# Kernel tuning notes

Hardware: AMD Instinct MI355X
Metric: run time of the kernel (lower is better)

Reference implementation:

```python
import jax, jax.numpy as jnp
import numpy as np

HIDDEN = 1024
HEADS = 16
HEAD_DIM = HIDDEN // HEADS


def setup_inputs() -> dict:
    key = jax.random.key(0)
    kx, kq, kk, kv, ko = jax.random.split(key, 5)
    s = 1.0 / np.sqrt(HIDDEN)
    return {
        "x": jax.random.normal(kx, (2, 2048, HIDDEN), dtype=jnp.float32),
        "Wq": jax.random.normal(kq, (HIDDEN, HIDDEN), dtype=jnp.float32) * s,
        "Wk": jax.random.normal(kk, (HIDDEN, HIDDEN), dtype=jnp.float32) * s,
        "Wv": jax.random.normal(kv, (HIDDEN, HIDDEN), dtype=jnp.float32) * s,
        "Wo": jax.random.normal(ko, (HIDDEN, HIDDEN), dtype=jnp.float32) * s,
    }


def reference(x, Wq, Wk, Wv, Wo):
    B, T, C = x.shape
    H, D = HEADS, HEAD_DIM
    # projections (torch Linear: y = x @ W.T); weights here stored as (out,in)==(C,C)
    q = (x @ Wq.T).reshape(B, T, H, D)
    k = (x @ Wk.T).reshape(B, T, H, D)
    v = (x @ Wv.T).reshape(B, T, H, D)
    scale = 1.0 / np.sqrt(D).astype(np.float32)
    # scores: (B,H,T,T)
    attn = jnp.einsum("bqhd,bkhd->bhqk", q, k) * scale
    causal = jnp.tril(jnp.ones((T, T), dtype=bool))  # keep lower triangle
    attn = jnp.where(causal, attn, -jnp.inf)
    attn = jax.nn.softmax(attn, axis=-1)
    out = jnp.einsum("bhqk,bkhd->bqhd", attn, v).reshape(B, T, C)
    return out @ Wo.T
```

## Files before the change

kernel.cpp:

```cpp
#include <hip/hip_runtime.h>
#include <cstdint>
#include <cstddef>

#define HID 1024
#define NH 16
#define HD 64
#define SEQ 2048
#define BATCH 2

typedef __attribute__((ext_vector_type(8))) short bf16x8;
typedef __attribute__((ext_vector_type(4))) short bf16x4;
typedef bf16x8 __attribute__((may_alias)) bf16x8_ma;
typedef bf16x4 __attribute__((may_alias)) bf16x4_ma;
typedef __attribute__((ext_vector_type(4))) float f32x4;

__device__ __forceinline__ unsigned short f2bf(float f){
  unsigned u = __builtin_bit_cast(unsigned, f);
  u += 0x7fffu + ((u >> 16) & 1u);
  return (unsigned short)(u >> 16);
}

__device__ __forceinline__ unsigned cvtpk_bf16(float lo, float hi){
  unsigned r;
  asm("v_cvt_pk_bf16_f32 %0, %1, %2" : "=v"(r) : "v"(lo), "v"(hi));
  return r;
}

__device__ __forceinline__ void gll(const unsigned short* g, unsigned short* l){
  __builtin_amdgcn_global_load_lds(
      (const __attribute__((address_space(1))) unsigned int*)(g),
      (__attribute__((address_space(3))) unsigned int*)(l),
      16, 0, 0);
}

__global__ __launch_bounds__(256) void cvt_all(
    const float* __restrict__ x,  const float* __restrict__ wq,
    const float* __restrict__ wk, const float* __restrict__ wv,
    const float* __restrict__ wo,
    unsigned short* __restrict__ xb,  unsigned short* __restrict__ wqb,
    unsigned short* __restrict__ wkb, unsigned short* __restrict__ wvb,
    unsigned short* __restrict__ wob)
{
  const size_t NX = (size_t)BATCH*SEQ*HID;
  const size_t NW = (size_t)HID*HID;
  size_t i = ((size_t)blockIdx.x*256 + threadIdx.x)*4;
  const float* src; unsigned short* dst; size_t off;
  if (i < NX) { src = x; dst = xb; off = i; }
  else {
    size_t j = i - NX; int w = (int)(j >> 20); off = j & (NW-1);
    if      (w==0){ src=wq; dst=wqb; }
    else if (w==1){ src=wk; dst=wkb; }
    else if (w==2){ src=wv; dst=wvb; }
    else          { src=wo; dst=wob; }
  }
  float4 v = *(const float4*)(src+off);
  uint2 p;
  p.x = (unsigned)f2bf(v.x) | ((unsigned)f2bf(v.y)<<16);
  p.y = (unsigned)f2bf(v.z) | ((unsigned)f2bf(v.w)<<16);
  *(uint2*)(dst+off) = p;
}

__global__ __launch_bounds__(256) void gemm_qkv(
    const unsigned short* __restrict__ A,
    const unsigned short* __restrict__ Bq,
    const unsigned short* __restrict__ Bk,
    const unsigned short* __restrict__ Bv,
    unsigned short* __restrict__ Qh,
    unsigned short* __restrict__ Kh,
    unsigned short* __restrict__ Vh)
{
  __shared__ unsigned short As[8192];
  __shared__ unsigned short Bs[8192];
  const int tid = threadIdx.x;
  const int w = tid >> 6, lane = tid & 63, l15 = lane & 15, quad = lane >> 4;
  const int wm = (w >> 1)*64, wn = (w & 1)*64;
  const int bm = blockIdx.y*128;
  const int which = blockIdx.x >> 3;
  const int bn = (blockIdx.x & 7)*128;
  const unsigned short* B = which==0 ? Bq : (which==1 ? Bk : Bv);
  unsigned short* C       = which==0 ? Qh : (which==1 ? Kh : Vh);
  const float cscale      = which==0 ? 0.18033688011112042f : 1.0f;
  const int lrow = lane >> 2, lcol = (lane & 3)*8;

  f32x4 acc[4][4] = {};
  for (int kb=0; kb<16; ++kb){
    __syncthreads();
    #pragma unroll
    for (int p=0;p<4;p++){
      int c = p*4 + w;
      int h = c >> 3, rb = c & 7;
      gll(&A[(size_t)(bm + rb*16 + lrow)*HID + kb*64 + h*32 + lcol], &As[h*4096 + rb*512]);
      gll(&B[(size_t)(bn + rb*16 + lrow)*HID + kb*64 + h*32 + lcol], &Bs[h*4096 + rb*512]);
    }
    __syncthreads();
    #pragma unroll
    for (int kc=0;kc<2;kc++){
      bf16x8 af[4], bfr[4];
      #pragma unroll
      for (int i=0;i<4;i++) af[i]  = *(const bf16x8*)(&As[kc*4096 + (wm + i*16 + l15)*32 + quad*8]);
      #pragma unroll
      for (int j=0;j<4;j++) bfr[j] = *(const bf16x8*)(&Bs[kc*4096 + (wn + j*16 + l15)*32 + quad*8]);
      #pragma unroll
      for (int i=0;i<4;i++)
        #pragma unroll
        for (int j=0;j<4;j++)
          acc[i][j] = __builtin_amdgcn_mfma_f32_16x16x32_bf16(af[i], bfr[j], acc[i][j], 0,0,0);
    }
  }
  #pragma unroll
  for (int i=0;i<4;i++)
    #pragma unroll
    for (int j=0;j<4;j++)
      #pragma unroll
      for (int r=0;r<4;r++){
        int m = bm + wm + i*16 + quad*4 + r;
        int n = bn + wn + j*16 + l15;
        int b = m >> 11, t = m & (SEQ-1), h = n >> 6, d = n & (HD-1);
        C[(((size_t)(b*NH + h))*SEQ + t)*HD + d] = f2bf(acc[i][j][r]*cscale);
      }
}

__global__ __launch_bounds__(256) void gemm_out(
    const unsigned short* __restrict__ A,
    const unsigned short* __restrict__ B,
    float* __restrict__ C)
{
  __shared__ unsigned short As[8192];
  __shared__ unsigned short Bs[4096];
  const int tid = threadIdx.x;
  const int w = tid >> 6, lane = tid & 63, l15 = lane & 15, quad = lane >> 4;
  const int wm = (w >> 1)*64, wn = (w & 1)*32;
  const int bm = blockIdx.y*128, bn = blockIdx.x*64;
  const int lrow = lane >> 2, lcol = (lane & 3)*8;

  f32x4 acc[4][2] = {};
  for (int kb=0; kb<16; ++kb){
    __syncthreads();
    #pragma unroll
    for (int p=0;p<4;p++){
      int c = p*4 + w;
      int h = c >> 3, rb = c & 7;
      gll(&A[(size_t)(bm + rb*16 + lrow)*HID + kb*64 + h*32 + lcol], &As[h*4096 + rb*512]);
    }
    #pragma unroll
    for (int p=0;p<2;p++){
      int c = p*4 + w;
      int h = c >> 2, rb = c & 3;
      gll(&B[(size_t)(bn + rb*16 + lrow)*HID + kb*64 + h*32 + lcol], &Bs[h*2048 + rb*512]);
    }
    __syncthreads();
    #pragma unroll
    for (int kc=0;kc<2;kc++){
      bf16x8 af[4], bfr[2];
      #pragma unroll
      for (int i=0;i<4;i++) af[i]  = *(const bf16x8*)(&As[kc*4096 + (wm + i*16 + l15)*32 + quad*8]);
      #pragma unroll
      for (int j=0;j<2;j++) bfr[j] = *(const bf16x8*)(&Bs[kc*2048 + (wn + j*16 + l15)*32 + quad*8]);
      #pragma unroll
      for (int i=0;i<4;i++)
        #pragma unroll
        for (int j=0;j<2;j++)
          acc[i][j] = __builtin_amdgcn_mfma_f32_16x16x32_bf16(af[i], bfr[j], acc[i][j], 0,0,0);
    }
  }
  #pragma unroll
  for (int i=0;i<4;i++)
    #pragma unroll
    for (int j=0;j<2;j++)
      #pragma unroll
      for (int r=0;r<4;r++){
        int m = bm + wm + i*16 + quad*4 + r;
        int n = bn + wn + j*16 + l15;
        C[(size_t)m*HID + n] = acc[i][j][r];
      }
}

__global__ __launch_bounds__(256) void vtrans(
    const unsigned short* __restrict__ Vh, unsigned short* __restrict__ VhT)
{
  __shared__ unsigned short t[64*66];
  const int bh = blockIdx.y, tb = blockIdx.x;
  const int tid = threadIdx.x;
  const unsigned short* src = Vh + ((size_t)bh*SEQ + tb*64)*HD;
  #pragma unroll
  for (int i=0;i<2;i++){
    int c = i*256 + tid; int r = c >> 3, c8 = (c & 7)*8;
    unsigned short tmp[8];
    *(uint4*)tmp = *(const uint4*)(&src[r*HD + c8]);
    #pragma unroll
    for (int j=0;j<8;j++) t[(c8+j)*66 + r] = tmp[j];
  }
  __syncthreads();
  unsigned short* dst = VhT + (size_t)bh*HD*SEQ + tb*64;
  #pragma unroll
  for (int i=0;i<2;i++){
    int c = i*256 + tid; int d = c >> 3, t8 = (c & 7)*8;
    uint4 v; unsigned short* pv = (unsigned short*)&v;
    #pragma unroll
    for (int j=0;j<8;j++) pv[j] = t[d*66 + t8 + j];
    *(uint4*)(&dst[(size_t)d*SEQ + t8]) = v;
  }
}

__global__ __launch_bounds__(256, 4) void attn(
    const unsigned short* __restrict__ Qh,
    const unsigned short* __restrict__ Kh,
    const unsigned short* __restrict__ VhT,
    unsigned short* __restrict__ Ao)
{
  __shared__ unsigned short QP[4096];
  __shared__ unsigned short Ks[2][4096];
  __shared__ unsigned short Vt[2][4096];

  const int bh = blockIdx.x;
  const int y  = blockIdx.y;
  const int a = y & 7, bb = y >> 3;
  const int qb = (bb & 1) ? (7 - a)*4 + bb : a*4 + bb;
  const int tid = threadIdx.x;
  const int w = tid >> 6, lane = tid & 63, l15 = lane & 15, quad = lane >> 4;
  const int lrow = lane >> 2, lcol = (lane & 3)*8;

  const size_t base = (size_t)bh * SEQ * HD;
  const unsigned short* Qg  = Qh + base + (size_t)qb*64*HD;
  const unsigned short* VTg = VhT + base;
  unsigned short* Psw = QP + w*1024;
  const unsigned swz = (unsigned)(l15 & 7) << 4;

  #pragma unroll
  for (int p=0;p<2;p++){
    int c = w*2 + p;
    gll(&Qg[(size_t)((c&3)*16 + lrow)*HD + (c>>2)*32 + lcol], &QP[(c>>2)*2048 + (c&3)*512]);
  }
  {
    const unsigned short* Kg = Kh + base;
    if (w < 2){
      #pragma unroll
      for (int p=0;p<4;p++){ int cc = w*4 + p;
        gll(&Kg[(size_t)((cc&3)*16 + lrow)*HD + (cc>>2)*32 + lcol], &Ks[0][(cc>>2)*2048 + (cc&3)*512]); }
    } else {
      #pragma unroll
      for (int p=0;p<4;p++){ int cc = (w-2)*4 + p;
        gll(&VTg[(size_t)((cc&3)*16 + lrow)*SEQ + (cc>>2)*32 + lcol], &Vt[0][(cc>>2)*2048 + (cc&3)*512]); }
    }
  }
  __syncthreads();
  bf16x8 qfrag[2];
  #pragma unroll
  for (int kc=0;kc<2;kc++)
    qfrag[kc] = *(const bf16x8*)(&QP[kc*2048 + (w*16 + l15)*32 + quad*8]);
  __syncthreads();

  f32x4 lacc = {0.f, 0.f, 0.f, 0.f};
  f32x4 oacc[4] = {};
  const int qrow = qb*64 + w*16 + l15;
  int cur = 0;

  for (int kb=0; kb<=qb; ++kb){
    if (kb < qb){
      const unsigned short* Kg2 = Kh + base + (size_t)(kb+1)*64*HD;
      unsigned short* Kd = Ks[cur^1];
      unsigned short* Vd = Vt[cur^1];
      if (w < 2){
        #pragma unroll
        for (int p=0;p<4;p++){ int cc = w*4 + p;
          gll(&Kg2[(size_t)((cc&3)*16 + lrow)*HD + (cc>>2)*32 + lcol], &Kd[(cc>>2)*2048 + (cc&3)*512]); }
      } else {
        #pragma unroll
        for (int p=0;p<4;p++){ int cc = (w-2)*4 + p;
          gll(&VTg[(size_t)((cc&3)*16 + lrow)*SEQ + (size_t)(kb+1)*64 + (cc>>2)*32 + lcol], &Vd[(cc>>2)*2048 + (cc&3)*512]); }
      }
    }

    const unsigned short* Ksc = Ks[cur];
    f32x4 s[4] = {};
    #pragma unroll
    for (int cb=0;cb<4;cb++)
      #pragma unroll
      for (int kc=0;kc<2;kc++){
        bf16x8 kfr = *(const bf16x8*)(&Ksc[kc*2048 + (cb*16 + l15)*32 + quad*8]);
        s[cb] = __builtin_amdgcn_mfma_f32_16x16x32_bf16(kfr, qfrag[kc], s[cb], 0,0,0);
      }

    if (kb == qb){
      #pragma unroll
      for (int cb=0;cb<4;cb++)
        #pragma unroll
        for (int r=0;r<4;r++){
          int t = kb*64 + cb*16 + quad*4 + r;
          if (t > qrow) s[cb][r] = -1e30f;
        }
    }
    #pragma unroll
    for (int cb=0;cb<4;cb++)
      #pragma unroll
      for (int r=0;r<4;r++)
        s[cb][r] = exp2f(s[cb][r]);
    lacc += (s[0] + s[1]) + (s[2] + s[3]);

    #pragma unroll
    for (int cb=0;cb<4;cb++){
      uint2 d2;
      d2.x = cvtpk_bf16(s[cb][0], s[cb][1]);
      d2.y = cvtpk_bf16(s[cb][2], s[cb][3]);
      *(bf16x4_ma*)((char*)Psw + (((unsigned)(l15*128 + cb*32 + quad*8)) ^ swz)) =
          __builtin_bit_cast(bf16x4, d2);
    }
    asm volatile("" ::: "memory");
    bf16x8 pa[2];
    #pragma unroll
    for (int kc=0;kc<2;kc++)
      pa[kc] = *(const bf16x8_ma*)((const char*)Psw + (((unsigned)(l15*128 + kc*64 + quad*16)) ^ swz));

    const unsigned short* Vtc = Vt[cur];
    #pragma unroll
    for (int db=0;db<4;db++)
      #pragma unroll
      for (int kc=0;kc<2;kc++){
        bf16x8 vfr = *(const bf16x8*)(&Vtc[kc*2048 + (db*16 + l15)*32 + quad*8]);
        oacc[db] = __builtin_amdgcn_mfma_f32_16x16x32_bf16(pa[kc], vfr, oacc[db], 0,0,0);
      }

    if (kb < qb) __syncthreads();
    cur ^= 1;
  }

  float l = (lacc[0] + lacc[1]) + (lacc[2] + lacc[3]);
  l += __shfl_xor(l, 16);
  l += __shfl_xor(l, 32);
  float inv[4];
  #pragma unroll
  for (int r=0;r<4;r++)
    inv[r] = 1.0f / __shfl(l, quad*4 + r);

  const int b = bh >> 4, h = bh & (NH-1);
  #pragma unroll
  for (int db=0;db<4;db++)
    #pragma unroll
    for (int r=0;r<4;r++){
      int t = qb*64 + w*16 + quad*4 + r;
      int col = h*HD + db*16 + l15;
      Ao[((size_t)b*SEQ + t)*HID + col] = f2bf(oacc[db][r] * inv[r]);
    }
}

extern "C" void kernel_launch(void* const* d_in, const int* in_sizes, int n_in,
                              void* d_out, int out_size, void* d_ws, size_t ws_size,
                              hipStream_t stream)
{
  const float* x  = (const float*)d_in[0];
  const float* Wq = (const float*)d_in[1];
  const float* Wk = (const float*)d_in[2];
  const float* Wv = (const float*)d_in[3];
  const float* Wo = (const float*)d_in[4];

  unsigned short* xb  = (unsigned short*)d_ws;
  unsigned short* wqb = xb  + (size_t)4*1024*1024;
  unsigned short* wkb = wqb + (size_t)1024*1024;
  unsigned short* wvb = wkb + (size_t)1024*1024;
  unsigned short* wob = wvb + (size_t)1024*1024;
  unsigned short* Qh  = wob + (size_t)1024*1024;
  unsigned short* Kh  = Qh  + (size_t)4*1024*1024;
  unsigned short* Vh  = Kh  + (size_t)4*1024*1024;
  unsigned short* VhT = Vh  + (size_t)4*1024*1024;
  unsigned short* Ao  = xb;

  cvt_all<<<8192, 256, 0, stream>>>(x, Wq, Wk, Wv, Wo, xb, wqb, wkb, wvb, wob);

  gemm_qkv<<<dim3(24, 32), 256, 0, stream>>>(xb, wqb, wkb, wvb, Qh, Kh, Vh);

  vtrans<<<dim3(SEQ/64, BATCH*NH), 256, 0, stream>>>(Vh, VhT);

  attn<<<dim3(BATCH*NH, SEQ/64), 256, 0, stream>>>(Qh, Kh, VhT, Ao);

  gemm_out<<<dim3(16, 32), 256, 0, stream>>>(Ao, wob, (float*)d_out);
}
```

Measured before the change: 188.8 us.

## Double-buffer QKV GEMM K-loop and stage epilogue through swizzled LDS

After: 181.3 us. 4.0% less time.

```diff
diff --git a/kernel.cpp b/kernel.cpp
--- a/kernel.cpp
+++ b/kernel.cpp
@@ -12,6 +12,7 @@
 typedef __attribute__((ext_vector_type(4))) short bf16x4;
 typedef bf16x8 __attribute__((may_alias)) bf16x8_ma;
 typedef bf16x4 __attribute__((may_alias)) bf16x4_ma;
+typedef uint4 __attribute__((may_alias)) uint4_ma;
 typedef __attribute__((ext_vector_type(4))) float f32x4;
 
 __device__ __forceinline__ unsigned short f2bf(float f){
@@ -69,8 +70,7 @@
     unsigned short* __restrict__ Kh,
     unsigned short* __restrict__ Vh)
 {
-  __shared__ unsigned short As[8192];
-  __shared__ unsigned short Bs[8192];
+  __shared__ unsigned short S[16384];
   const int tid = threadIdx.x;
   const int w = tid >> 6, lane = tid & 63, l15 = lane & 15, quad = lane >> 4;
   const int wm = (w >> 1)*64, wn = (w & 1)*64;
@@ -83,41 +83,69 @@
   const int lrow = lane >> 2, lcol = (lane & 3)*8;
 
   f32x4 acc[4][4] = {};
-  for (int kb=0; kb<16; ++kb){
+
+  {
+    #pragma unroll
+    for (int p=0;p<2;p++){
+      int c = w*2 + p;
+      gll(&A[(size_t)(bm + c*16 + lrow)*HID + lcol], &S[c*512]);
+      gll(&B[(size_t)(bn + c*16 + lrow)*HID + lcol], &S[8192 + c*512]);
+    }
+  }
+  __syncthreads();
+
+  int cur = 0;
+  for (int kb=0; kb<32; ++kb){
+    if (kb < 31){
+      unsigned short* Ad = S + (cur^1)*4096;
+      unsigned short* Bd = S + 8192 + (cur^1)*4096;
+      #pragma unroll
+      for (int p=0;p<2;p++){
+        int c = w*2 + p;
+        gll(&A[(size_t)(bm + c*16 + lrow)*HID + (kb+1)*32 + lcol], &Ad[c*512]);
+        gll(&B[(size_t)(bn + c*16 + lrow)*HID + (kb+1)*32 + lcol], &Bd[c*512]);
+      }
+    }
+    const unsigned short* Ac = S + cur*4096;
+    const unsigned short* Bc = S + 8192 + cur*4096;
+    bf16x8 af[4], bfr[4];
+    #pragma unroll
+    for (int i=0;i<4;i++) af[i]  = *(const bf16x8*)(&Ac[(wm + i*16 + l15)*32 + quad*8]);
+    #pragma unroll
+    for (int j=0;j<4;j++) bfr[j] = *(const bf16x8*)(&Bc[(wn + j*16 + l15)*32 + quad*8]);
+    #pragma unroll
+    for (int i=0;i<4;i++)
+      #pragma unroll
+      for (int j=0;j<4;j++)
+        acc[i][j] = __builtin_amdgcn_mfma_f32_16x16x32_bf16(af[i], bfr[j], acc[i][j], 0,0,0);
     __syncthreads();
-    #pragma unroll
-    for (int p=0;p<4;p++){
-      int c = p*4 + w;
-      int h = c >> 3, rb = c & 7;
-      gll(&A[(size_t)(bm + rb*16 + lrow)*HID + kb*64 + h*32 + lcol], &As[h*4096 + rb*512]);
-      gll(&B[(size_t)(bn + rb*16 + lrow)*HID + kb*64 + h*32 + lcol], &Bs[h*4096 + rb*512]);
-    }
-    __syncthreads();
-    #pragma unroll
-    for (int kc=0;kc<2;kc++){
-      bf16x8 af[4], bfr[4];
-      #pragma unroll
-      for (int i=0;i<4;i++) af[i]  = *(const bf16x8*)(&As[kc*4096 + (wm + i*16 + l15)*32 + quad*8]);
-      #pragma unroll
-      for (int j=0;j<4;j++) bfr[j] = *(const bf16x8*)(&Bs[kc*4096 + (wn + j*16 + l15)*32 + quad*8]);
-      #pragma unroll
-      for (int i=0;i<4;i++)
-        #pragma unroll
-        for (int j=0;j<4;j++)
-          acc[i][j] = __builtin_amdgcn_mfma_f32_16x16x32_bf16(af[i], bfr[j], acc[i][j], 0,0,0);
-    }
-  }
+    cur ^= 1;
+  }
+
   #pragma unroll
   for (int i=0;i<4;i++)
     #pragma unroll
     for (int j=0;j<4;j++)
       #pragma unroll
       for (int r=0;r<4;r++){
-        int m = bm + wm + i*16 + quad*4 + r;
-        int n = bn + wn + j*16 + l15;
-        int b = m >> 11, t = m & (SEQ-1), h = n >> 6, d = n & (HD-1);
-        C[(((size_t)(b*NH + h))*SEQ + t)*HD + d] = f2bf(acc[i][j][r]*cscale);
-      }
+        int row = wm + i*16 + quad*4 + r;
+        int col = wn + j*16 + l15;
+        unsigned off = (unsigned)(row*256 + col*2);
+        *(unsigned short*)((char*)S + (off ^ ((unsigned)(row & 7) << 4))) =
+            f2bf(acc[i][j][r]*cscale);
+      }
+  __syncthreads();
+  #pragma unroll
+  for (int pass=0; pass<8; ++pass){
+    int tr    = pass*16 + (tid >> 4);
+    int half  = (tid >> 3) & 1;
+    int blkin = tid & 7;
+    unsigned off = (unsigned)(tr*256 + half*128 + blkin*16);
+    uint4 v = *(const uint4_ma*)((const char*)S + (off ^ ((unsigned)(tr & 7) << 4)));
+    int m = bm + tr, b = m >> 11, t = m & (SEQ-1);
+    int h = (bn >> 6) + half;
+    *(uint4*)(&C[(((size_t)(b*NH + h))*SEQ + t)*HD + blkin*8]) = v;
+  }
 }
 
 __global__ __launch_bounds__(256) void gemm_out(
```
